# Performance work log

Measured on AMD Instinct MI355X. Metric: run time of the kernel, lower is better.

## Reference

```python
import jax, jax.numpy as jnp
import numpy as np

N, A, H, W = 8, 256, 128, 128
C = 19            # number of real classes (fc rows)
CP1 = 20          # estimator classes = class_num + 1
HT, WT = 1024, 1024


def setup_inputs() -> dict:
    key = jax.random.key(0)
    k1, k2, k3, k4 = jax.random.split(key, 4)
    return {
        "features": jax.random.normal(k1, (N, A, H, W), dtype=jnp.float32),
        "y": jax.random.normal(k2, (N, C, H, W), dtype=jnp.float32),
        "fc_weight": jax.random.normal(k3, (C, A), dtype=jnp.float32) * 0.05,
        "Ave": jnp.zeros((CP1, A), jnp.float32),
        "CoVariance": jnp.zeros((CP1, A), jnp.float32),
        "Amount": jnp.zeros((CP1,), jnp.float32),
        "target": jax.random.randint(k4, (N, HT, WT), 0, C, dtype=jnp.int64),
        "ratio": 5,
    }


def reference(features, y, fc_weight, Ave, CoVariance, Amount, target, ratio):
    n, a, h, w = features.shape
    ht, wt = target.shape[1], target.shape[2]
    # nearest-neighbor downsample of labels: src_idx = floor(dst * in/out)
    ih = (jnp.arange(h) * ht) // h
    iw = (jnp.arange(w) * wt) // w
    tgt = target[:, ih][:, :, iw]                       # [N,H,W]

    feats = features.transpose(0, 2, 3, 1).reshape(-1, a)   # [NHW, A]
    y2 = y.transpose(0, 2, 3, 1).reshape(-1, C)              # [NHW, C]
    labels = tgt.reshape(-1)                                  # [NHW]

    mask255 = labels == 255
    lab0 = jnp.where(mask255, 0, labels)                      # 255 -> 0

    # ---- EstimatorCV.update_CV: per-class scatter mean / variance ----
    f = jax.lax.stop_gradient(feats)
    counts = jnp.zeros((CP1,), f.dtype).at[lab0].add(1.0)     # [CP1]
    counts_c = jnp.where(counts == 0, 1.0, counts)
    sums = jnp.zeros((CP1, a), f.dtype).at[lab0].add(f)
    ave = sums / counts_c[:, None]                            # [CP1, A]
    var = jnp.zeros((CP1, a), f.dtype).at[lab0].add((f - ave[lab0]) ** 2)
    var = var / counts_c[:, None]

    denom = counts + Amount
    wcv = jnp.where(denom > 0, counts / denom, 0.0)[:, None]  # [CP1,1]
    new_cov = CoVariance * (1 - wcv) + var * wcv + wcv * (1 - wcv) * (Ave - ave) ** 2
    new_cov = jax.lax.stop_gradient(new_cov)                  # .detach() in torch

    # ---- isda_aug: sigma2[n,c] = ratio * sum_a (W[c]-W[l_n])^2 * CV[l_n] ----
    Wm = fc_weight                                            # [C, A]
    CVl = new_cov[lab0]                                       # [NHW, A]
    Wl = Wm[lab0]                                             # [NHW, A]
    sigma2 = ratio * (
        CVl @ (Wm ** 2).T
        - 2.0 * (CVl * Wl) @ Wm.T
        + jnp.sum(Wl ** 2 * CVl, axis=-1, keepdims=True)
    )                                                          # [NHW, C]

    keep = (1.0 - mask255.astype(y2.dtype))[:, None]
    aug = y2 + 0.5 * sigma2 * keep
    return aug.reshape(n, h, w, C).transpose(0, 3, 1, 2)
```

## Files before the change

kernel.cpp:

```cpp
#include <hip/hip_runtime.h>

#define NB   8
#define AB   256
#define HB   128
#define WB   128
#define CB   19
#define CP1  20
#define PLANE (HB*WB)
#define NPIX  (NB*PLANE)

__global__ __launch_bounds__(256) void k_labels(const int* __restrict__ target,
                                                unsigned char* __restrict__ labels,
                                                float* __restrict__ counts) {
    __shared__ int hist[CP1];
    int tid = threadIdx.x;
    if (tid < CP1) hist[tid] = 0;
    __syncthreads();

    int p = blockIdx.x * 256 + tid;
    int n   = p >> 14;
    int rem = p & 16383;
    int h   = rem >> 7;
    int w   = rem & 127;
    size_t idx = (size_t)n * 1048576 + (size_t)h * 8192 + (size_t)w * 8;
    int l = target[idx];
    labels[p] = (unsigned char)l;
    int lab0 = (l == 255) ? 0 : l;
    if (lab0 < 0 || lab0 >= CP1) lab0 = 0;
    atomicAdd(&hist[lab0], 1);
    __syncthreads();
    if (tid < CP1) atomicAdd(&counts[tid], (float)hist[tid]);
}

__global__ __launch_bounds__(256) void k_stats(const float* __restrict__ features,
                                               const unsigned char* __restrict__ labels,
                                               float* __restrict__ gsum,
                                               float* __restrict__ gsq) {
    __shared__ float acc[CP1 * 256 * 2];
    int tid = threadIdx.x;
    int a = blockIdx.x & 255;
    int n = blockIdx.x >> 8;

    for (int i = tid; i < CP1 * 256 * 2; i += 256) acc[i] = 0.f;
    __syncthreads();

    const float* fbase = features + ((size_t)(n * AB + a)) * PLANE;
    const unsigned char* lbase = labels + (size_t)n * PLANE;

    #pragma unroll 4
    for (int it = 0; it < 16; ++it) {
        int pix = it * 1024 + tid * 4;
        float4 f = *reinterpret_cast<const float4*>(fbase + pix);
        unsigned int lw = *reinterpret_cast<const unsigned int*>(lbase + pix);
        float fa[4] = {f.x, f.y, f.z, f.w};
        #pragma unroll
        for (int j = 0; j < 4; ++j) {
            int l = (lw >> (8 * j)) & 255;
            int lab0 = (l == 255) ? 0 : (l < CP1 ? l : 0);
            int b = (lab0 * 256 + tid) * 2;
            float v = fa[j];
            acc[b]     += v;
            acc[b + 1] += v * v;
        }
    }
    __syncthreads();

    #pragma unroll
    for (int off = 128; off >= 1; off >>= 1) {
        for (int idx = tid; idx < CP1 * off; idx += 256) {
            int l = idx / off;
            int j = idx - l * off;
            int b0 = (l * 256 + j) * 2;
            int b1 = (l * 256 + j + off) * 2;
            acc[b0]     += acc[b1];
            acc[b0 + 1] += acc[b1 + 1];
        }
        __syncthreads();
    }

    if (tid < CP1) {
        atomicAdd(&gsum[tid * 256 + a], acc[tid * 512]);
        atomicAdd(&gsq [tid * 256 + a], acc[tid * 512 + 1]);
    }
}

__global__ __launch_bounds__(256) void k_table(const float* __restrict__ counts,
                                               const float* __restrict__ gsum,
                                               const float* __restrict__ gsq,
                                               const float* __restrict__ fcw,
                                               const float* __restrict__ Ave,
                                               const float* __restrict__ CoV,
                                               const float* __restrict__ Amount,
                                               const int* __restrict__ ratio_p,
                                               float* __restrict__ table) {
    __shared__ float ncov_s[256];
    __shared__ float wl_s[256];
    __shared__ float red[4];
    int t = threadIdx.x;
    int l = blockIdx.x;

    float cnt  = counts[l];
    float cntc = (cnt == 0.f) ? 1.f : cnt;
    float sum  = gsum[l * 256 + t];
    float sq   = gsq [l * 256 + t];
    float ave  = sum / cntc;
    float var  = sq / cntc - ave * ave;
    float denom = cnt + Amount[l];
    float wcv  = (denom > 0.f) ? cnt / denom : 0.f;
    float d0   = Ave[l * 256 + t] - ave;
    float ncov = CoV[l * 256 + t] * (1.f - wcv) + var * wcv + wcv * (1.f - wcv) * d0 * d0;

    ncov_s[t] = ncov;
    int lw = (l < CB) ? l : (CB - 1);
    wl_s[t] = fcw[lw * 256 + t];
    __syncthreads();

    float ratio_f = (float)(*ratio_p);
    for (int c = 0; c < CB; ++c) {
        float dv = fcw[c * 256 + t] - wl_s[t];
        float r = ncov_s[t] * dv * dv;
        #pragma unroll
        for (int off = 32; off; off >>= 1) r += __shfl_down(r, off);
        if ((t & 63) == 0) red[t >> 6] = r;
        __syncthreads();
        if (t == 0) table[l * CB + c] = ratio_f * (red[0] + red[1] + red[2] + red[3]);
        __syncthreads();
    }
}

__global__ __launch_bounds__(256) void k_apply(const float* __restrict__ y,
                                               const unsigned char* __restrict__ labels,
                                               const float* __restrict__ table,
                                               float* __restrict__ out) {
    __shared__ float tab[CP1 * CB];
    int tid = threadIdx.x;
    for (int i = tid; i < CP1 * CB; i += 256) tab[i] = table[i];
    __syncthreads();

    int b = blockIdx.x;
    int chunk = b & 3;
    int c = (b >> 2) % CB;
    int n = b / (4 * CB);

    const float* ybase = y + ((size_t)(n * CB + c)) * PLANE;
    float* obase = out + ((size_t)(n * CB + c)) * PLANE;
    const unsigned char* lbase = labels + (size_t)n * PLANE;

    #pragma unroll
    for (int it = 0; it < 4; ++it) {
        int pix = chunk * 4096 + it * 1024 + tid * 4;
        float4 yv = *reinterpret_cast<const float4*>(ybase + pix);
        unsigned int lw = *reinterpret_cast<const unsigned int*>(lbase + pix);
        float ya[4] = {yv.x, yv.y, yv.z, yv.w};
        float o[4];
        #pragma unroll
        for (int j = 0; j < 4; ++j) {
            int l = (lw >> (8 * j)) & 255;
            bool keep = (l != 255);
            int lab0 = keep ? (l < CP1 ? l : 0) : 0;
            float s = tab[lab0 * CB + c];
            o[j] = ya[j] + (keep ? 0.5f * s : 0.f);
        }
        *reinterpret_cast<float4*>(obase + pix) = make_float4(o[0], o[1], o[2], o[3]);
    }
}

extern "C" void kernel_launch(void* const* d_in, const int* in_sizes, int n_in,
                              void* d_out, int out_size, void* d_ws, size_t ws_size,
                              hipStream_t stream) {
    const float* features = (const float*)d_in[0];
    const float* y        = (const float*)d_in[1];
    const float* fcw      = (const float*)d_in[2];
    const float* Ave      = (const float*)d_in[3];
    const float* CoV      = (const float*)d_in[4];
    const float* Amount   = (const float*)d_in[5];
    const int*   target   = (const int*)d_in[6];
    const int*   ratio    = (const int*)d_in[7];

    char* ws = (char*)d_ws;
    float* counts = (float*)(ws + 0);
    float* gsum   = (float*)(ws + 128);
    float* gsq    = (float*)(ws + 20608);
    unsigned char* labels = (unsigned char*)(ws + 41088);
    float* table  = (float*)(ws + 41088 + 131072);
    float* out    = (float*)d_out;

    hipMemsetAsync(ws, 0, 41088, stream);

    k_labels<<<NPIX / 256, 256, 0, stream>>>(target, labels, counts);
    k_stats <<<NB * AB,     256, 0, stream>>>(features, labels, gsum, gsq);
    k_table <<<CP1,         256, 0, stream>>>(counts, gsum, gsq, fcw, Ave, CoV, Amount, ratio, table);
    k_apply <<<NB * CB * 4, 256, 0, stream>>>(y, labels, table, out);
}
```

Before: 249.1 us.

## Pipeline feature loads via global_load_lds and shrink shared stats accumulators

The stats kernel now splits each plane across two blocks. It stages feature loads through a triple-buffered direct global-to-LDS pipeline with explicit vmcnt waits, and it accumulates with LDS atomics into a 128-column accumulator instead of per-thread slots. This cuts shared memory so more blocks fit per CU, shortens the tree reduction, and overlaps memory latency with compute. The table kernel now assigns one class per wavefront and drops its block-wide syncs. Risks: LDS atomic contention between threads sharing a column, and the hand-written vmcnt waits must match the actual number of outstanding loads.

```diff
diff --git a/kernel.cpp b/kernel.cpp
--- a/kernel.cpp
+++ b/kernel.cpp
@@ -1,4 +1,5 @@
 #include <hip/hip_runtime.h>
+#include <stdint.h>
 
 #define NB   8
 #define AB   256
@@ -36,51 +37,79 @@
                                                const unsigned char* __restrict__ labels,
                                                float* __restrict__ gsum,
                                                float* __restrict__ gsq) {
-    __shared__ float acc[CP1 * 256 * 2];
-    int tid = threadIdx.x;
-    int a = blockIdx.x & 255;
-    int n = blockIdx.x >> 8;
-
-    for (int i = tid; i < CP1 * 256 * 2; i += 256) acc[i] = 0.f;
-    __syncthreads();
-
-    const float* fbase = features + ((size_t)(n * AB + a)) * PLANE;
-    const unsigned char* lbase = labels + (size_t)n * PLANE;
-
-    #pragma unroll 4
-    for (int it = 0; it < 16; ++it) {
-        int pix = it * 1024 + tid * 4;
-        float4 f = *reinterpret_cast<const float4*>(fbase + pix);
-        unsigned int lw = *reinterpret_cast<const unsigned int*>(lbase + pix);
+    __shared__ float acc[CP1 * 2 * 128];
+    __shared__ float fbuf[3][4][256];
+
+    const int tid  = threadIdx.x;
+    const int lane = tid & 63;
+    const int w    = tid >> 6;
+    const int col  = tid & 127;
+
+    for (int i = tid; i < CP1 * 2 * 128; i += 256) acc[i] = 0.f;
+
+    const int b    = blockIdx.x;
+    const int half = b & 1;
+    const int a    = (b >> 1) & 255;
+    const int n    = b >> 9;
+
+    const float* fsrc = features + ((size_t)(n * AB + a)) * PLANE
+                        + half * 8192 + w * 2048 + lane * 4;
+    const uint32_t* lsrc = (const uint32_t*)(labels + (size_t)n * PLANE + half * 8192)
+                           + w * 512 + lane;
+
+    uint32_t lw[8];
+    #pragma unroll
+    for (int it = 0; it < 8; ++it) lw[it] = lsrc[it * 64];
+
+    __syncthreads();
+
+    #define STAGE(IT, BUF)                                                        \
+        __builtin_amdgcn_global_load_lds(                                         \
+            (const __attribute__((address_space(1))) void*)(fsrc + (IT) * 256),   \
+            (__attribute__((address_space(3))) void*)(&fbuf[BUF][w][lane * 4]),   \
+            16, 0, 0)
+
+    STAGE(0, 0);
+    STAGE(1, 1);
+
+    #pragma unroll
+    for (int it = 0; it < 8; ++it) {
+        if (it + 2 < 8) STAGE(it + 2, (it + 2) % 3);
+        if (it < 6)      asm volatile("s_waitcnt vmcnt(2)" ::: "memory");
+        else if (it == 6) asm volatile("s_waitcnt vmcnt(1)" ::: "memory");
+        else              asm volatile("s_waitcnt vmcnt(0)" ::: "memory");
+
+        float4 f = *(const float4*)&fbuf[it % 3][w][lane * 4];
+        uint32_t lwv = lw[it];
         float fa[4] = {f.x, f.y, f.z, f.w};
         #pragma unroll
         for (int j = 0; j < 4; ++j) {
-            int l = (lw >> (8 * j)) & 255;
-            int lab0 = (l == 255) ? 0 : (l < CP1 ? l : 0);
-            int b = (lab0 * 256 + tid) * 2;
+            int l = (lwv >> (8 * j)) & 255;
+            l = (l >= CP1) ? 0 : l;
             float v = fa[j];
-            acc[b]     += v;
-            acc[b + 1] += v * v;
+            atomicAdd(&acc[l * 256 + col], v);
+            atomicAdd(&acc[l * 256 + 128 + col], v * v);
         }
     }
-    __syncthreads();
-
-    #pragma unroll
-    for (int off = 128; off >= 1; off >>= 1) {
-        for (int idx = tid; idx < CP1 * off; idx += 256) {
-            int l = idx / off;
-            int j = idx - l * off;
-            int b0 = (l * 256 + j) * 2;
-            int b1 = (l * 256 + j + off) * 2;
-            acc[b0]     += acc[b1];
-            acc[b0 + 1] += acc[b1 + 1];
+    #undef STAGE
+
+    __syncthreads();
+
+    #pragma unroll
+    for (int off = 64; off >= 1; off >>= 1) {
+        for (int i = tid; i < CP1 * 2 * off; i += 256) {
+            int cs = i / off;
+            int j  = i - cs * off;
+            acc[cs * 128 + j] += acc[cs * 128 + j + off];
         }
         __syncthreads();
     }
 
-    if (tid < CP1) {
-        atomicAdd(&gsum[tid * 256 + a], acc[tid * 512]);
-        atomicAdd(&gsq [tid * 256 + a], acc[tid * 512 + 1]);
+    if (tid < CP1 * 2) {
+        float v = acc[tid * 128];
+        int l = tid >> 1, s = tid & 1;
+        float* dst = s ? gsq : gsum;
+        atomicAdd(&dst[l * 256 + a], v);
     }
 }
 
@@ -95,7 +124,6 @@
                                                float* __restrict__ table) {
     __shared__ float ncov_s[256];
     __shared__ float wl_s[256];
-    __shared__ float red[4];
     int t = threadIdx.x;
     int l = blockIdx.x;
 
@@ -111,20 +139,21 @@
     float ncov = CoV[l * 256 + t] * (1.f - wcv) + var * wcv + wcv * (1.f - wcv) * d0 * d0;
 
     ncov_s[t] = ncov;
-    int lw = (l < CB) ? l : (CB - 1);
-    wl_s[t] = fcw[lw * 256 + t];
-    __syncthreads();
-
+    int lwr = (l < CB) ? l : (CB - 1);
+    wl_s[t] = fcw[lwr * 256 + t];
+    __syncthreads();
+
+    int wv = t >> 6, lane = t & 63;
     float ratio_f = (float)(*ratio_p);
-    for (int c = 0; c < CB; ++c) {
-        float dv = fcw[c * 256 + t] - wl_s[t];
-        float r = ncov_s[t] * dv * dv;
+    for (int c = wv; c < CB; c += 4) {
+        float4 nc = *(const float4*)&ncov_s[lane * 4];
+        float4 wl = *(const float4*)&wl_s[lane * 4];
+        float4 wc = *(const float4*)&fcw[c * 256 + lane * 4];
+        float e0 = wc.x - wl.x, e1 = wc.y - wl.y, e2 = wc.z - wl.z, e3 = wc.w - wl.w;
+        float r = nc.x * e0 * e0 + nc.y * e1 * e1 + nc.z * e2 * e2 + nc.w * e3 * e3;
         #pragma unroll
         for (int off = 32; off; off >>= 1) r += __shfl_down(r, off);
-        if ((t & 63) == 0) red[t >> 6] = r;
-        __syncthreads();
-        if (t == 0) table[l * CB + c] = ratio_f * (red[0] + red[1] + red[2] + red[3]);
-        __syncthreads();
+        if (lane == 0) table[l * CB + c] = ratio_f * r;
     }
 }
 
@@ -150,12 +179,12 @@
     for (int it = 0; it < 4; ++it) {
         int pix = chunk * 4096 + it * 1024 + tid * 4;
         float4 yv = *reinterpret_cast<const float4*>(ybase + pix);
-        unsigned int lw = *reinterpret_cast<const unsigned int*>(lbase + pix);
+        unsigned int lwv = *reinterpret_cast<const unsigned int*>(lbase + pix);
         float ya[4] = {yv.x, yv.y, yv.z, yv.w};
         float o[4];
         #pragma unroll
         for (int j = 0; j < 4; ++j) {
-            int l = (lw >> (8 * j)) & 255;
+            int l = (lwv >> (8 * j)) & 255;
             bool keep = (l != 255);
             int lab0 = keep ? (l < CP1 ? l : 0) : 0;
             float s = tab[lab0 * CB + c];
@@ -187,8 +216,8 @@
 
     hipMemsetAsync(ws, 0, 41088, stream);
 
-    k_labels<<<NPIX / 256, 256, 0, stream>>>(target, labels, counts);
-    k_stats <<<NB * AB,     256, 0, stream>>>(features, labels, gsum, gsq);
+    k_labels<<<NPIX / 256,  256, 0, stream>>>(target, labels, counts);
+    k_stats <<<NB * AB * 2, 256, 0, stream>>>(features, labels, gsum, gsq);
     k_table <<<CP1,         256, 0, stream>>>(counts, gsum, gsq, fcw, Ave, CoV, Amount, ratio, table);
     k_apply <<<NB * CB * 4, 256, 0, stream>>>(y, labels, table, out);
 }
```

Measured after the change: 541.8 us. 2.18x slower.
